# Optimization experiments

Measured on AMD Instinct MI355X. Metric: run time of the kernel, lower is better.

The kernel has to match this reference:

```python
import jax, jax.numpy as jnp
import numpy as np

LOG2 = float(np.log(2.0))


def setup_inputs() -> dict:
    key = jax.random.key(0)
    ks = jax.random.split(key, 10)
    V, G, F, T = 262144, 4096, 256, 2
    node_feats = jax.random.normal(ks[0], (V, F), dtype=jnp.float32)
    segment_ids = jnp.sort(jax.random.randint(ks[1], (V,), 0, G))
    s = 0.05
    return {
        "node_feats": node_feats,
        "segment_ids": segment_ids,
        "num_graphs": G,
        "logit_w": jax.random.normal(ks[2], (T, 2 * F, 1), dtype=jnp.float32) * s,
        "logit_b": jnp.zeros((T, 1), dtype=jnp.float32),
        "proj_w": jax.random.normal(ks[3], (T, F, F), dtype=jnp.float32) * s,
        "proj_b": jnp.zeros((T, F), dtype=jnp.float32),
        "gru_w_ih": jax.random.normal(ks[4], (T, 3 * F, F), dtype=jnp.float32) * s,
        "gru_w_hh": jax.random.normal(ks[5], (T, 3 * F, F), dtype=jnp.float32) * s,
        "gru_b_ih": jnp.zeros((T, 3 * F), dtype=jnp.float32),
        "gru_b_hh": jnp.zeros((T, 3 * F), dtype=jnp.float32),
    }


def _gru_cell(x, h, w_ih, w_hh, b_ih, b_hh):
    # torch.nn.GRUCell math
    gi = x @ w_ih.T + b_ih  # [G, 3F]
    gh = h @ w_hh.T + b_hh
    i_r, i_z, i_n = jnp.split(gi, 3, axis=-1)
    h_r, h_z, h_n = jnp.split(gh, 3, axis=-1)
    r = jax.nn.sigmoid(i_r + h_r)
    z = jax.nn.sigmoid(i_z + h_z)
    n = jnp.tanh(i_n + r * h_n)
    return (1.0 - z) * n + z * h


def reference(node_feats, segment_ids, num_graphs, logit_w, logit_b,
              proj_w, proj_b, gru_w_ih, gru_w_hh, gru_b_ih, gru_b_hh):
    G = int(num_graphs)
    # initial graph feats: sum of node feats per graph
    g_feats = jax.ops.segment_sum(node_feats, segment_ids, num_segments=G)
    T = logit_w.shape[0]
    for t in range(T):
        # broadcast relu(g_feats) to nodes, concat with node feats, compute logits
        ctx_nodes = jax.nn.relu(g_feats)[segment_ids]              # [V, F]
        z = jnp.concatenate([ctx_nodes, node_feats], axis=-1) @ logit_w[t] + logit_b[t]  # [V,1]
        z = jnp.logaddexp(z, 0.0) - LOG2                           # SoftPlus2
        # segment softmax over nodes within each graph
        zmax = jax.ops.segment_max(z, segment_ids, num_segments=G)
        e = jnp.exp(z - zmax[segment_ids])
        denom = jax.ops.segment_sum(e, segment_ids, num_segments=G)
        a = e / denom[segment_ids]                                 # [V,1]
        # project nodes (dropout=0) and attention-weighted sum per graph
        hv = node_feats @ proj_w[t] + proj_b[t]                    # [V, F]
        g_repr = jax.ops.segment_sum(a * hv, segment_ids, num_segments=G)
        context = jax.nn.elu(g_repr)
        g_feats = _gru_cell(context, g_feats, gru_w_ih[t], gru_w_hh[t], gru_b_ih[t], gru_b_hh[t])
    return g_feats
```

## Files before the change

### kernel.cpp

```cpp
#include <hip/hip_runtime.h>
#include <hip/hip_bf16.h>
#include <math.h>

#define V_NODES 262144
#define NGRAPH  4096
#define FD      256
#define TSTEPS  2
#define GP      16
#define SB      512
#define RS      264

typedef unsigned short u16;
typedef __attribute__((ext_vector_type(8))) short short8;
typedef __attribute__((ext_vector_type(4))) float f32x4;

__device__ __forceinline__ float bf2f(u16 u) {
  union { unsigned int i; float f; } x; x.i = ((unsigned int)u) << 16; return x.f;
}
__device__ __forceinline__ u16 f2bf(float f) {
  union { unsigned int i; float f; } x; x.f = f;
  unsigned int r = x.i + 0x7FFFu + ((x.i >> 16) & 1u);
  return (u16)(r >> 16);
}
__device__ __forceinline__ unsigned int pkbf(float a, float b) {
  return (unsigned int)f2bf(a) | ((unsigned int)f2bf(b) << 16);
}
__device__ __forceinline__ float softplus2(float x) {
  return fmaxf(x, 0.0f) + log1pf(__expf(-fabsf(x))) - 0.69314718056f;
}

__global__ __launch_bounds__(256) void k_prep(
    const int* __restrict__ seg, const float* __restrict__ w_ih,
    const float* __restrict__ w_hh, const float* __restrict__ proj_w,
    int* __restrict__ start, u16* __restrict__ wihbf, u16* __restrict__ whhbf,
    u16* __restrict__ whhlo, u16* __restrict__ pwtbf) {
  __shared__ float tl[32][33];
  const int b = blockIdx.x, tid = threadIdx.x;
  const int gtid = b * 256 + tid;
  {
    const int v = gtid;
    const int s = seg[v];
    if (v == 0) {
      for (int g = 0; g <= s; ++g) start[g] = 0;
    } else {
      const int p = seg[v - 1];
      for (int g = p + 1; g <= s; ++g) start[g] = v;
    }
    if (v == V_NODES - 1)
      for (int g = s + 1; g <= NGRAPH; ++g) start[g] = V_NODES;
  }
  {
    const int nchunk = TSTEPS * 768 * FD / 4;
    if (gtid < nchunk) {
      const float4 x = ((const float4*)w_ih)[gtid];
      uint2 u; u.x = pkbf(x.x, x.y); u.y = pkbf(x.z, x.w);
      ((uint2*)wihbf)[gtid] = u;
      const float4 y = ((const float4*)w_hh)[gtid];
      const u16 h0 = f2bf(y.x), h1 = f2bf(y.y), h2 = f2bf(y.z), h3 = f2bf(y.w);
      uint2 hi_, lo_;
      hi_.x = (unsigned)h0 | ((unsigned)h1 << 16);
      hi_.y = (unsigned)h2 | ((unsigned)h3 << 16);
      lo_.x = pkbf(y.x - bf2f(h0), y.y - bf2f(h1));
      lo_.y = pkbf(y.z - bf2f(h2), y.w - bf2f(h3));
      ((uint2*)whhbf)[gtid] = hi_;
      ((uint2*)whhlo)[gtid] = lo_;
    }
  }
  if (b < 2 * 64) {
    const int t = b >> 6, tile = b & 63, bx = tile & 7, by = tile >> 3;
    const int tx = tid & 31, ty = tid >> 5;
    const float* S = proj_w + (size_t)t * FD * FD;
    u16* D = pwtbf + (size_t)t * FD * FD;
#pragma unroll
    for (int i = 0; i < 32; i += 8)
      tl[ty + i][tx] = S[(size_t)(by * 32 + ty + i) * FD + bx * 32 + tx];
    __syncthreads();
#pragma unroll
    for (int i = 0; i < 32; i += 8)
      D[(size_t)(bx * 32 + ty + i) * FD + by * 32 + tx] = f2bf(tl[tx][ty + i]);
  }
}

__global__ __launch_bounds__(256) void k_pass1(
    const float* __restrict__ nf, const int* __restrict__ start,
    const float* __restrict__ logit_w, float* __restrict__ gf,
    u16* __restrict__ nbf, float* __restrict__ d0, float* __restrict__ d1) {
  __shared__ __align__(16) float redf[8][FD];
  const int g = blockIdx.x, tid = threadIdx.x;
  const int h = tid >> 5, sl = tid & 31;
  const int s = start[g], e = start[g + 1];
  float wA[8], wB[8];
  {
    const float4 a0 = ((const float4*)(logit_w + FD))[2 * sl];
    const float4 a1 = ((const float4*)(logit_w + FD))[2 * sl + 1];
    const float4 b0 = ((const float4*)(logit_w + 512 + FD))[2 * sl];
    const float4 b1 = ((const float4*)(logit_w + 512 + FD))[2 * sl + 1];
    wA[0]=a0.x; wA[1]=a0.y; wA[2]=a0.z; wA[3]=a0.w;
    wA[4]=a1.x; wA[5]=a1.y; wA[6]=a1.z; wA[7]=a1.w;
    wB[0]=b0.x; wB[1]=b0.y; wB[2]=b0.z; wB[3]=b0.w;
    wB[4]=b1.x; wB[5]=b1.y; wB[6]=b1.z; wB[7]=b1.w;
  }
  float ac[8];
#pragma unroll
  for (int j = 0; j < 8; ++j) ac[j] = 0.f;
  const float4* nfv = (const float4*)nf;
  for (int v = s + h; v < e; v += 8) {
    const float4 x0 = nfv[(size_t)v * 64 + 2 * sl];
    const float4 x1 = nfv[(size_t)v * 64 + 2 * sl + 1];
    ac[0]+=x0.x; ac[1]+=x0.y; ac[2]+=x0.z; ac[3]+=x0.w;
    ac[4]+=x1.x; ac[5]+=x1.y; ac[6]+=x1.z; ac[7]+=x1.w;
    uint4 u;
    u.x = pkbf(x0.x, x0.y); u.y = pkbf(x0.z, x0.w);
    u.z = pkbf(x1.x, x1.y); u.w = pkbf(x1.z, x1.w);
    ((uint4*)(nbf + (size_t)v * FD))[sl] = u;
    float dA = fmaf(x0.x, wA[0], fmaf(x0.y, wA[1], fmaf(x0.z, wA[2], x0.w * wA[3])));
    dA = fmaf(x1.x, wA[4], fmaf(x1.y, wA[5], fmaf(x1.z, wA[6], fmaf(x1.w, wA[7], dA))));
    float dB = fmaf(x0.x, wB[0], fmaf(x0.y, wB[1], fmaf(x0.z, wB[2], x0.w * wB[3])));
    dB = fmaf(x1.x, wB[4], fmaf(x1.y, wB[5], fmaf(x1.z, wB[6], fmaf(x1.w, wB[7], dB))));
#pragma unroll
    for (int off = 1; off < 32; off <<= 1) {
      dA += __shfl_xor(dA, off, 64);
      dB += __shfl_xor(dB, off, 64);
    }
    if (sl == 0) { d0[v] = dA; d1[v] = dB; }
  }
  ((float4*)&redf[h][sl * 8])[0] = make_float4(ac[0], ac[1], ac[2], ac[3]);
  ((float4*)&redf[h][sl * 8])[1] = make_float4(ac[4], ac[5], ac[6], ac[7]);
  __syncthreads();
  float sum = 0.f;
#pragma unroll
  for (int j = 0; j < 8; ++j) sum += redf[j][tid];
  gf[(size_t)g * FD + tid] = sum;
}

__global__ __launch_bounds__(SB, 1) void k_steps(
    const int* __restrict__ start, const float* __restrict__ logit_w,
    const float* __restrict__ logit_b, const float* __restrict__ proj_b,
    const float* __restrict__ b_ih, const float* __restrict__ b_hh,
    const u16* __restrict__ nbf, const float* __restrict__ d0,
    const float* __restrict__ d1, float* __restrict__ gf,
    float* __restrict__ gibuf, float* __restrict__ ghbuf,
    const u16* __restrict__ wihbf, const u16* __restrict__ whhbf,
    const u16* __restrict__ whhlo, const u16* __restrict__ pwtbf) {
  __shared__ __align__(16) float ew[2560];
  __shared__ __align__(16) float redf[GP * FD];
  __shared__ __align__(16) u16 wns_s[GP * RS];
  __shared__ __align__(16) u16 ctx_s[GP * RS];
  __shared__ __align__(16) u16 hhi_s[GP * RS];
  __shared__ __align__(16) u16 hlo_s[GP * RS];
  const int b = blockIdx.x, tid = threadIdx.x;
  const int lane = tid & 63, wv = tid >> 6;
  const int half = lane >> 5, sl = lane & 31;
  const int g0 = b * GP;
  const int vs = start[g0];
  const int hw = wv * 2 + half;
  const int g = g0 + hw;
  const int s = start[g], e = start[g + 1];

  for (int t = 0; t < TSTEPS; ++t) {
    for (int i = tid; i < GP * FD; i += SB) {
      const float x = gf[(size_t)g0 * FD + i];
      const u16 hb = f2bf(x);
      const int row = i >> 8, f = i & 255;
      hhi_s[row * RS + f] = hb;
      hlo_s[row * RS + f] = f2bf(x - bf2f(hb));
    }
    __syncthreads();
    {
      const float lb = logit_b[t];
      const float* dt = t ? d1 : d0;
      const float* lwA = logit_w + (size_t)t * 512;
      const float4 h0 = ((const float4*)(gf + (size_t)g * FD))[2 * sl];
      const float4 h1 = ((const float4*)(gf + (size_t)g * FD))[2 * sl + 1];
      const float4 wa0 = ((const float4*)lwA)[2 * sl];
      const float4 wa1 = ((const float4*)lwA)[2 * sl + 1];
      float c = fmaf(fmaxf(h0.x, 0.f), wa0.x, fmaf(fmaxf(h0.y, 0.f), wa0.y,
                fmaf(fmaxf(h0.z, 0.f), wa0.z, fmaxf(h0.w, 0.f) * wa0.w)));
      c = fmaf(fmaxf(h1.x, 0.f), wa1.x, fmaf(fmaxf(h1.y, 0.f), wa1.y,
          fmaf(fmaxf(h1.z, 0.f), wa1.z, fmaf(fmaxf(h1.w, 0.f), wa1.w, c))));
#pragma unroll
      for (int off = 1; off < 32; off <<= 1) c += __shfl_xor(c, off, 64);
      float m = -1e30f;
      for (int v = s + sl; v < e; v += 32) {
        const float z = softplus2(c + dt[v] + lb);
        ew[v - vs] = z;
        m = fmaxf(m, z);
      }
#pragma unroll
      for (int off = 1; off < 32; off <<= 1) m = fmaxf(m, __shfl_xor(m, off, 64));
      float ls = 0.f;
      for (int v = s + sl; v < e; v += 32) {
        const float ezz = __expf(ew[v - vs] - m);
        ew[v - vs] = ezz;
        ls += ezz;
      }
#pragma unroll
      for (int off = 1; off < 32; off <<= 1) ls += __shfl_xor(ls, off, 64);
      const float inv = (e > s) ? 1.0f / ls : 0.f;
      for (int v = s + sl; v < e; v += 32) ew[v - vs] *= inv;
      float acc[8];
#pragma unroll
      for (int j = 0; j < 8; ++j) acc[j] = 0.f;
      for (int v = s; v < e; ++v) {
        const uint4 u = ((const uint4*)(nbf + (size_t)v * FD))[sl];
        const float a = ew[v - vs];
        acc[0] = fmaf(a, bf2f((u16)(u.x & 0xffff)), acc[0]);
        acc[1] = fmaf(a, bf2f((u16)(u.x >> 16)),    acc[1]);
        acc[2] = fmaf(a, bf2f((u16)(u.y & 0xffff)), acc[2]);
        acc[3] = fmaf(a, bf2f((u16)(u.y >> 16)),    acc[3]);
        acc[4] = fmaf(a, bf2f((u16)(u.z & 0xffff)), acc[4]);
        acc[5] = fmaf(a, bf2f((u16)(u.z >> 16)),    acc[5]);
        acc[6] = fmaf(a, bf2f((u16)(u.w & 0xffff)), acc[6]);
        acc[7] = fmaf(a, bf2f((u16)(u.w >> 16)),    acc[7]);
      }
      ((float4*)&redf[hw * FD + sl * 8])[0] = make_float4(acc[0], acc[1], acc[2], acc[3]);
      ((float4*)&redf[hw * FD + sl * 8])[1] = make_float4(acc[4], acc[5], acc[6], acc[7]);
    }
    __syncthreads();
    for (int i = tid; i < GP * FD; i += SB)
      wns_s[(i >> 8) * RS + (i & 255)] = f2bf(redf[i]);
    __syncthreads();
    {
      const int r = lane & 15, q = lane >> 4;
      const u16* xp = wns_s + r * RS + q * 8;
#pragma unroll
      for (int jj = 0; jj < 2; ++jj) {
        const int nt = wv * 2 + jj;
        const u16* wp = pwtbf + (size_t)t * FD * FD + (size_t)(nt * 16 + r) * FD + q * 8;
        f32x4 a4 = {0.f, 0.f, 0.f, 0.f};
#pragma unroll
        for (int kt = 0; kt < 8; ++kt) {
          const short8 av = *(const short8*)(xp + kt * 32);
          const short8 bv = *(const short8*)(wp + kt * 32);
          a4 = __builtin_amdgcn_mfma_f32_16x16x32_bf16(av, bv, a4, 0, 0, 0);
        }
        const int gcol = nt * 16 + r;
        const float bs = proj_b[t * FD + gcol];
#pragma unroll
        for (int i = 0; i < 4; ++i) {
          float v = a4[i] + bs;
          v = (v > 0.0f) ? v : expm1f(v);
          ctx_s[(q * 4 + i) * RS + gcol] = f2bf(v);
        }
      }
    }
    __syncthreads();
    {
      const int r = lane & 15, q = lane >> 4;
      const u16* wih_t = wihbf + (size_t)t * 768 * FD;
      const u16* whh_t = whhbf + (size_t)t * 768 * FD;
      const u16* whl_t = whhlo + (size_t)t * 768 * FD;
      const u16* xi = ctx_s + r * RS + q * 8;
      const u16* xh = hhi_s + r * RS + q * 8;
      const u16* xl = hlo_s + r * RS + q * 8;
#pragma unroll
      for (int j = 0; j < 6; ++j) {
        const int nt = wv * 6 + j;
        const int gcol = nt * 16 + r;
        const u16* wi = wih_t + (size_t)gcol * FD + q * 8;
        const u16* wh = whh_t + (size_t)gcol * FD + q * 8;
        const u16* wl = whl_t + (size_t)gcol * FD + q * 8;
        f32x4 ai = {0.f, 0.f, 0.f, 0.f};
        f32x4 ah = {0.f, 0.f, 0.f, 0.f};
#pragma unroll
        for (int kt = 0; kt < 8; ++kt) {
          const short8 bi = *(const short8*)(wi + kt * 32);
          const short8 aiv = *(const short8*)(xi + kt * 32);
          ai = __builtin_amdgcn_mfma_f32_16x16x32_bf16(aiv, bi, ai, 0, 0, 0);
          const short8 bh = *(const short8*)(wh + kt * 32);
          const short8 xhh = *(const short8*)(xh + kt * 32);
          const short8 xll = *(const short8*)(xl + kt * 32);
          ah = __builtin_amdgcn_mfma_f32_16x16x32_bf16(xhh, bh, ah, 0, 0, 0);
          ah = __builtin_amdgcn_mfma_f32_16x16x32_bf16(xll, bh, ah, 0, 0, 0);
          const short8 bl = *(const short8*)(wl + kt * 32);
          ah = __builtin_amdgcn_mfma_f32_16x16x32_bf16(xhh, bl, ah, 0, 0, 0);
        }
        const float bi_ = b_ih[t * 768 + gcol];
        const float bh_ = b_hh[t * 768 + gcol];
#pragma unroll
        for (int i = 0; i < 4; ++i) {
          gibuf[(size_t)(g0 + q * 4 + i) * 768 + gcol] = ai[i] + bi_;
          ghbuf[(size_t)(g0 + q * 4 + i) * 768 + gcol] = ah[i] + bh_;
        }
      }
    }
    __syncthreads();
    for (int i = tid; i < GP * FD; i += SB) {
      const int lg = i >> 8, f = i & 255;
      const size_t gr = (size_t)(g0 + lg) * 768;
      const float ir = gibuf[gr + f], iz = gibuf[gr + 256 + f], in_ = gibuf[gr + 512 + f];
      const float hr = ghbuf[gr + f], hz = ghbuf[gr + 256 + f], hn = ghbuf[gr + 512 + f];
      const float rr = 1.0f / (1.0f + __expf(-(ir + hr)));
      const float zz = 1.0f / (1.0f + __expf(-(iz + hz)));
      const float nn = tanhf(in_ + rr * hn);
      const size_t idx = (size_t)g0 * FD + i;
      gf[idx] = (1.0f - zz) * nn + zz * gf[idx];
    }
    __syncthreads();
  }
}

extern "C" void kernel_launch(void* const* d_in, const int* in_sizes, int n_in,
                              void* d_out, int out_size, void* d_ws, size_t ws_size,
                              hipStream_t stream) {
  const float* node    = (const float*)d_in[0];
  const int*   seg     = (const int*)d_in[1];
  const float* logit_w = (const float*)d_in[3];
  const float* logit_b = (const float*)d_in[4];
  const float* proj_w  = (const float*)d_in[5];
  const float* proj_b  = (const float*)d_in[6];
  const float* w_ih    = (const float*)d_in[7];
  const float* w_hh    = (const float*)d_in[8];
  const float* b_ih    = (const float*)d_in[9];
  const float* b_hh    = (const float*)d_in[10];
  float* gfeats = (float*)d_out;

  char* p = (char*)d_ws;
  int* start   = (int*)p;   p += (((NGRAPH + 1) * sizeof(int)) + 255) & ~(size_t)255;
  u16* nbf     = (u16*)p;   p += (size_t)V_NODES * FD * 2;
  float* d0    = (float*)p; p += (size_t)V_NODES * 4;
  float* d1    = (float*)p; p += (size_t)V_NODES * 4;
  float* gi    = (float*)p; p += (size_t)NGRAPH * 768 * 4;
  float* gh    = (float*)p; p += (size_t)NGRAPH * 768 * 4;
  u16* wihbf   = (u16*)p;   p += (size_t)TSTEPS * 768 * FD * 2;
  u16* whhbf   = (u16*)p;   p += (size_t)TSTEPS * 768 * FD * 2;
  u16* whhlo   = (u16*)p;   p += (size_t)TSTEPS * 768 * FD * 2;
  u16* pwtbf   = (u16*)p;   p += (size_t)TSTEPS * FD * FD * 2;
  (void)ws_size; (void)in_sizes; (void)n_in; (void)out_size;

  k_prep<<<dim3(V_NODES / 256), dim3(256), 0, stream>>>(
      seg, w_ih, w_hh, proj_w, start, wihbf, whhbf, whhlo, pwtbf);
  k_pass1<<<dim3(NGRAPH), dim3(256), 0, stream>>>(
      node, start, logit_w, gfeats, nbf, d0, d1);
  k_steps<<<dim3(NGRAPH / GP), dim3(SB), 0, stream>>>(
      start, logit_w, logit_b, proj_b, b_ih, b_hh, nbf, d0, d1,
      gfeats, gi, gh, wihbf, whhbf, whhlo, pwtbf);
}
```

Before: 596.5 us.

## Fuse pass1 into step kernel, keep graph state and logits in LDS

Merges the node-sum/bf16-conversion pass into the step kernel so each block handles 8 graphs end to end. Graph features, per-node logit dot products and GRU results stay in shared memory instead of round-tripping through global d0/d1, gi/gh and gf buffers. The GRU gate elementwise math is fused directly into the MFMA epilogue, and node loops are unrolled by two. The group size is halved (MFMA rows padded with zeros) and occupancy raised, at the cost of wasted MFMA rows and a fixed LDS capacity for nodes per block.

```diff
diff --git a/kernel.cpp b/kernel.cpp
--- a/kernel.cpp
+++ b/kernel.cpp
@@ -6,9 +6,10 @@
 #define NGRAPH  4096
 #define FD      256
 #define TSTEPS  2
-#define GP      16
+#define GP      8
 #define SB      512
 #define RS      264
+#define EWCAP   1536
 
 typedef unsigned short u16;
 typedef __attribute__((ext_vector_type(8))) short short8;
@@ -27,6 +28,10 @@
 }
 __device__ __forceinline__ float softplus2(float x) {
   return fmaxf(x, 0.0f) + log1pf(__expf(-fabsf(x))) - 0.69314718056f;
+}
+__device__ __forceinline__ float dot8(const float4 x0, const float4 x1, const float* w) {
+  float d = fmaf(x0.x, w[0], fmaf(x0.y, w[1], fmaf(x0.z, w[2], x0.w * w[3])));
+  return fmaf(x1.x, w[4], fmaf(x1.y, w[5], fmaf(x1.z, w[6], fmaf(x1.w, w[7], d))));
 }
 
 __global__ __launch_bounds__(256) void k_prep(
@@ -81,144 +86,185 @@
   }
 }
 
-__global__ __launch_bounds__(256) void k_pass1(
+__global__ __launch_bounds__(SB, 4) void k_main(
     const float* __restrict__ nf, const int* __restrict__ start,
-    const float* __restrict__ logit_w, float* __restrict__ gf,
-    u16* __restrict__ nbf, float* __restrict__ d0, float* __restrict__ d1) {
-  __shared__ __align__(16) float redf[8][FD];
-  const int g = blockIdx.x, tid = threadIdx.x;
-  const int h = tid >> 5, sl = tid & 31;
-  const int s = start[g], e = start[g + 1];
-  float wA[8], wB[8];
-  {
-    const float4 a0 = ((const float4*)(logit_w + FD))[2 * sl];
-    const float4 a1 = ((const float4*)(logit_w + FD))[2 * sl + 1];
-    const float4 b0 = ((const float4*)(logit_w + 512 + FD))[2 * sl];
-    const float4 b1 = ((const float4*)(logit_w + 512 + FD))[2 * sl + 1];
-    wA[0]=a0.x; wA[1]=a0.y; wA[2]=a0.z; wA[3]=a0.w;
-    wA[4]=a1.x; wA[5]=a1.y; wA[6]=a1.z; wA[7]=a1.w;
-    wB[0]=b0.x; wB[1]=b0.y; wB[2]=b0.z; wB[3]=b0.w;
-    wB[4]=b1.x; wB[5]=b1.y; wB[6]=b1.z; wB[7]=b1.w;
-  }
-  float ac[8];
-#pragma unroll
-  for (int j = 0; j < 8; ++j) ac[j] = 0.f;
-  const float4* nfv = (const float4*)nf;
-  for (int v = s + h; v < e; v += 8) {
-    const float4 x0 = nfv[(size_t)v * 64 + 2 * sl];
-    const float4 x1 = nfv[(size_t)v * 64 + 2 * sl + 1];
-    ac[0]+=x0.x; ac[1]+=x0.y; ac[2]+=x0.z; ac[3]+=x0.w;
-    ac[4]+=x1.x; ac[5]+=x1.y; ac[6]+=x1.z; ac[7]+=x1.w;
-    uint4 u;
-    u.x = pkbf(x0.x, x0.y); u.y = pkbf(x0.z, x0.w);
-    u.z = pkbf(x1.x, x1.y); u.w = pkbf(x1.z, x1.w);
-    ((uint4*)(nbf + (size_t)v * FD))[sl] = u;
-    float dA = fmaf(x0.x, wA[0], fmaf(x0.y, wA[1], fmaf(x0.z, wA[2], x0.w * wA[3])));
-    dA = fmaf(x1.x, wA[4], fmaf(x1.y, wA[5], fmaf(x1.z, wA[6], fmaf(x1.w, wA[7], dA))));
-    float dB = fmaf(x0.x, wB[0], fmaf(x0.y, wB[1], fmaf(x0.z, wB[2], x0.w * wB[3])));
-    dB = fmaf(x1.x, wB[4], fmaf(x1.y, wB[5], fmaf(x1.z, wB[6], fmaf(x1.w, wB[7], dB))));
-#pragma unroll
-    for (int off = 1; off < 32; off <<= 1) {
-      dA += __shfl_xor(dA, off, 64);
-      dB += __shfl_xor(dB, off, 64);
-    }
-    if (sl == 0) { d0[v] = dA; d1[v] = dB; }
-  }
-  ((float4*)&redf[h][sl * 8])[0] = make_float4(ac[0], ac[1], ac[2], ac[3]);
-  ((float4*)&redf[h][sl * 8])[1] = make_float4(ac[4], ac[5], ac[6], ac[7]);
-  __syncthreads();
-  float sum = 0.f;
-#pragma unroll
-  for (int j = 0; j < 8; ++j) sum += redf[j][tid];
-  gf[(size_t)g * FD + tid] = sum;
-}
-
-__global__ __launch_bounds__(SB, 1) void k_steps(
-    const int* __restrict__ start, const float* __restrict__ logit_w,
-    const float* __restrict__ logit_b, const float* __restrict__ proj_b,
-    const float* __restrict__ b_ih, const float* __restrict__ b_hh,
-    const u16* __restrict__ nbf, const float* __restrict__ d0,
-    const float* __restrict__ d1, float* __restrict__ gf,
-    float* __restrict__ gibuf, float* __restrict__ ghbuf,
-    const u16* __restrict__ wihbf, const u16* __restrict__ whhbf,
-    const u16* __restrict__ whhlo, const u16* __restrict__ pwtbf) {
-  __shared__ __align__(16) float ew[2560];
-  __shared__ __align__(16) float redf[GP * FD];
-  __shared__ __align__(16) u16 wns_s[GP * RS];
-  __shared__ __align__(16) u16 ctx_s[GP * RS];
-  __shared__ __align__(16) u16 hhi_s[GP * RS];
-  __shared__ __align__(16) u16 hlo_s[GP * RS];
+    const float* __restrict__ logit_w, const float* __restrict__ logit_b,
+    const float* __restrict__ proj_b, const float* __restrict__ b_ih,
+    const float* __restrict__ b_hh, u16* __restrict__ nbf,
+    float* __restrict__ gf_out, const u16* __restrict__ wihbf,
+    const u16* __restrict__ whhbf, const u16* __restrict__ whhlo,
+    const u16* __restrict__ pwtbf) {
+  __shared__ __align__(16) float gf_s[GP][FD];
+  __shared__ __align__(16) float ew[EWCAP];
+  __shared__ __align__(16) float2 dle[EWCAP];
+  __shared__ __align__(16) u16 wns_s[16 * RS];
+  __shared__ __align__(16) u16 ctx_s[16 * RS];
+  __shared__ __align__(16) u16 hhi_s[16 * RS];
+  __shared__ __align__(16) u16 hlo_s[16 * RS];
+
   const int b = blockIdx.x, tid = threadIdx.x;
-  const int lane = tid & 63, wv = tid >> 6;
+  const int wv = tid >> 6, lane = tid & 63;
   const int half = lane >> 5, sl = lane & 31;
   const int g0 = b * GP;
+  const int g = g0 + wv;
   const int vs = start[g0];
-  const int hw = wv * 2 + half;
-  const int g = g0 + hw;
   const int s = start[g], e = start[g + 1];
+
+  for (int i = tid; i < 8 * RS; i += SB) {
+    wns_s[8 * RS + i] = 0; ctx_s[8 * RS + i] = 0;
+    hhi_s[8 * RS + i] = 0; hlo_s[8 * RS + i] = 0;
+  }
+
+  {
+    float wA[8], wB[8];
+    {
+      const float4 a0 = ((const float4*)(logit_w + FD))[2 * sl];
+      const float4 a1 = ((const float4*)(logit_w + FD))[2 * sl + 1];
+      const float4 b0 = ((const float4*)(logit_w + 512 + FD))[2 * sl];
+      const float4 b1 = ((const float4*)(logit_w + 512 + FD))[2 * sl + 1];
+      wA[0]=a0.x; wA[1]=a0.y; wA[2]=a0.z; wA[3]=a0.w;
+      wA[4]=a1.x; wA[5]=a1.y; wA[6]=a1.z; wA[7]=a1.w;
+      wB[0]=b0.x; wB[1]=b0.y; wB[2]=b0.z; wB[3]=b0.w;
+      wB[4]=b1.x; wB[5]=b1.y; wB[6]=b1.z; wB[7]=b1.w;
+    }
+    float ac[8];
+#pragma unroll
+    for (int j = 0; j < 8; ++j) ac[j] = 0.f;
+    const float4* nfv = (const float4*)nf;
+    int v = s + half;
+    for (; v + 2 < e; v += 4) {
+      const float4 x0 = nfv[(size_t)v * 64 + 2 * sl];
+      const float4 x1 = nfv[(size_t)v * 64 + 2 * sl + 1];
+      const float4 y0 = nfv[(size_t)(v + 2) * 64 + 2 * sl];
+      const float4 y1 = nfv[(size_t)(v + 2) * 64 + 2 * sl + 1];
+      uint4 u0, u1;
+      u0.x = pkbf(x0.x, x0.y); u0.y = pkbf(x0.z, x0.w);
+      u0.z = pkbf(x1.x, x1.y); u0.w = pkbf(x1.z, x1.w);
+      ((uint4*)(nbf + (size_t)v * FD))[sl] = u0;
+      u1.x = pkbf(y0.x, y0.y); u1.y = pkbf(y0.z, y0.w);
+      u1.z = pkbf(y1.x, y1.y); u1.w = pkbf(y1.z, y1.w);
+      ((uint4*)(nbf + (size_t)(v + 2) * FD))[sl] = u1;
+      ac[0] += x0.x + y0.x; ac[1] += x0.y + y0.y;
+      ac[2] += x0.z + y0.z; ac[3] += x0.w + y0.w;
+      ac[4] += x1.x + y1.x; ac[5] += x1.y + y1.y;
+      ac[6] += x1.z + y1.z; ac[7] += x1.w + y1.w;
+      float dA0 = dot8(x0, x1, wA), dB0 = dot8(x0, x1, wB);
+      float dA1 = dot8(y0, y1, wA), dB1 = dot8(y0, y1, wB);
+#pragma unroll
+      for (int off = 1; off < 32; off <<= 1) {
+        dA0 += __shfl_xor(dA0, off, 64); dB0 += __shfl_xor(dB0, off, 64);
+        dA1 += __shfl_xor(dA1, off, 64); dB1 += __shfl_xor(dB1, off, 64);
+      }
+      if (sl == 0) {
+        dle[v - vs] = make_float2(dA0, dB0);
+        dle[v + 2 - vs] = make_float2(dA1, dB1);
+      }
+    }
+    if (v < e) {
+      const float4 x0 = nfv[(size_t)v * 64 + 2 * sl];
+      const float4 x1 = nfv[(size_t)v * 64 + 2 * sl + 1];
+      uint4 u0;
+      u0.x = pkbf(x0.x, x0.y); u0.y = pkbf(x0.z, x0.w);
+      u0.z = pkbf(x1.x, x1.y); u0.w = pkbf(x1.z, x1.w);
+      ((uint4*)(nbf + (size_t)v * FD))[sl] = u0;
+      ac[0] += x0.x; ac[1] += x0.y; ac[2] += x0.z; ac[3] += x0.w;
+      ac[4] += x1.x; ac[5] += x1.y; ac[6] += x1.z; ac[7] += x1.w;
+      float dA0 = dot8(x0, x1, wA), dB0 = dot8(x0, x1, wB);
+#pragma unroll
+      for (int off = 1; off < 32; off <<= 1) {
+        dA0 += __shfl_xor(dA0, off, 64); dB0 += __shfl_xor(dB0, off, 64);
+      }
+      if (sl == 0) dle[v - vs] = make_float2(dA0, dB0);
+    }
+#pragma unroll
+    for (int j = 0; j < 8; ++j) ac[j] += __shfl_xor(ac[j], 32, 64);
+    if (half == 0) {
+      ((float4*)&gf_s[wv][sl * 8])[0] = make_float4(ac[0], ac[1], ac[2], ac[3]);
+      ((float4*)&gf_s[wv][sl * 8])[1] = make_float4(ac[4], ac[5], ac[6], ac[7]);
+    }
+  }
+  __syncthreads();
 
   for (int t = 0; t < TSTEPS; ++t) {
     for (int i = tid; i < GP * FD; i += SB) {
-      const float x = gf[(size_t)g0 * FD + i];
+      const float x = gf_s[i >> 8][i & 255];
       const u16 hb = f2bf(x);
-      const int row = i >> 8, f = i & 255;
-      hhi_s[row * RS + f] = hb;
-      hlo_s[row * RS + f] = f2bf(x - bf2f(hb));
-    }
-    __syncthreads();
+      hhi_s[(i >> 8) * RS + (i & 255)] = hb;
+      hlo_s[(i >> 8) * RS + (i & 255)] = f2bf(x - bf2f(hb));
+    }
     {
       const float lb = logit_b[t];
-      const float* dt = t ? d1 : d0;
-      const float* lwA = logit_w + (size_t)t * 512;
-      const float4 h0 = ((const float4*)(gf + (size_t)g * FD))[2 * sl];
-      const float4 h1 = ((const float4*)(gf + (size_t)g * FD))[2 * sl + 1];
-      const float4 wa0 = ((const float4*)lwA)[2 * sl];
-      const float4 wa1 = ((const float4*)lwA)[2 * sl + 1];
-      float c = fmaf(fmaxf(h0.x, 0.f), wa0.x, fmaf(fmaxf(h0.y, 0.f), wa0.y,
-                fmaf(fmaxf(h0.z, 0.f), wa0.z, fmaxf(h0.w, 0.f) * wa0.w)));
-      c = fmaf(fmaxf(h1.x, 0.f), wa1.x, fmaf(fmaxf(h1.y, 0.f), wa1.y,
-          fmaf(fmaxf(h1.z, 0.f), wa1.z, fmaf(fmaxf(h1.w, 0.f), wa1.w, c))));
-#pragma unroll
-      for (int off = 1; off < 32; off <<= 1) c += __shfl_xor(c, off, 64);
+      const float4 h4 = ((const float4*)&gf_s[wv][0])[lane];
+      const float4 w4 = ((const float4*)(logit_w + (size_t)t * 512))[lane];
+      float c = fmaf(fmaxf(h4.x, 0.f), w4.x, fmaf(fmaxf(h4.y, 0.f), w4.y,
+                fmaf(fmaxf(h4.z, 0.f), w4.z, fmaxf(h4.w, 0.f) * w4.w)));
+#pragma unroll
+      for (int off = 1; off < 64; off <<= 1) c += __shfl_xor(c, off, 64);
       float m = -1e30f;
-      for (int v = s + sl; v < e; v += 32) {
-        const float z = softplus2(c + dt[v] + lb);
-        ew[v - vs] = z;
+      for (int v2 = s + lane; v2 < e; v2 += 64) {
+        const float2 dd = dle[v2 - vs];
+        const float z = softplus2(c + (t ? dd.y : dd.x) + lb);
+        ew[v2 - vs] = z;
         m = fmaxf(m, z);
       }
 #pragma unroll
-      for (int off = 1; off < 32; off <<= 1) m = fmaxf(m, __shfl_xor(m, off, 64));
+      for (int off = 1; off < 64; off <<= 1) m = fmaxf(m, __shfl_xor(m, off, 64));
       float ls = 0.f;
-      for (int v = s + sl; v < e; v += 32) {
-        const float ezz = __expf(ew[v - vs] - m);
-        ew[v - vs] = ezz;
-        ls += ezz;
-      }
-#pragma unroll
-      for (int off = 1; off < 32; off <<= 1) ls += __shfl_xor(ls, off, 64);
+      for (int v2 = s + lane; v2 < e; v2 += 64) {
+        const float ez = __expf(ew[v2 - vs] - m);
+        ew[v2 - vs] = ez;
+        ls += ez;
+      }
+#pragma unroll
+      for (int off = 1; off < 64; off <<= 1) ls += __shfl_xor(ls, off, 64);
       const float inv = (e > s) ? 1.0f / ls : 0.f;
-      for (int v = s + sl; v < e; v += 32) ew[v - vs] *= inv;
+      for (int v2 = s + lane; v2 < e; v2 += 64) ew[v2 - vs] *= inv;
       float acc[8];
 #pragma unroll
       for (int j = 0; j < 8; ++j) acc[j] = 0.f;
-      for (int v = s; v < e; ++v) {
-        const uint4 u = ((const uint4*)(nbf + (size_t)v * FD))[sl];
-        const float a = ew[v - vs];
-        acc[0] = fmaf(a, bf2f((u16)(u.x & 0xffff)), acc[0]);
-        acc[1] = fmaf(a, bf2f((u16)(u.x >> 16)),    acc[1]);
-        acc[2] = fmaf(a, bf2f((u16)(u.y & 0xffff)), acc[2]);
-        acc[3] = fmaf(a, bf2f((u16)(u.y >> 16)),    acc[3]);
-        acc[4] = fmaf(a, bf2f((u16)(u.z & 0xffff)), acc[4]);
-        acc[5] = fmaf(a, bf2f((u16)(u.z >> 16)),    acc[5]);
-        acc[6] = fmaf(a, bf2f((u16)(u.w & 0xffff)), acc[6]);
-        acc[7] = fmaf(a, bf2f((u16)(u.w >> 16)),    acc[7]);
-      }
-      ((float4*)&redf[hw * FD + sl * 8])[0] = make_float4(acc[0], acc[1], acc[2], acc[3]);
-      ((float4*)&redf[hw * FD + sl * 8])[1] = make_float4(acc[4], acc[5], acc[6], acc[7]);
-    }
-    __syncthreads();
-    for (int i = tid; i < GP * FD; i += SB)
-      wns_s[(i >> 8) * RS + (i & 255)] = f2bf(redf[i]);
+      int v = s + half;
+      for (; v + 2 < e; v += 4) {
+        const uint4 u0 = ((const uint4*)(nbf + (size_t)v * FD))[sl];
+        const uint4 u1 = ((const uint4*)(nbf + (size_t)(v + 2) * FD))[sl];
+        const float a0 = ew[v - vs], a1 = ew[v + 2 - vs];
+        acc[0] = fmaf(a0, bf2f((u16)(u0.x & 0xffff)), acc[0]);
+        acc[1] = fmaf(a0, bf2f((u16)(u0.x >> 16)),    acc[1]);
+        acc[2] = fmaf(a0, bf2f((u16)(u0.y & 0xffff)), acc[2]);
+        acc[3] = fmaf(a0, bf2f((u16)(u0.y >> 16)),    acc[3]);
+        acc[4] = fmaf(a0, bf2f((u16)(u0.z & 0xffff)), acc[4]);
+        acc[5] = fmaf(a0, bf2f((u16)(u0.z >> 16)),    acc[5]);
+        acc[6] = fmaf(a0, bf2f((u16)(u0.w & 0xffff)), acc[6]);
+        acc[7] = fmaf(a0, bf2f((u16)(u0.w >> 16)),    acc[7]);
+        acc[0] = fmaf(a1, bf2f((u16)(u1.x & 0xffff)), acc[0]);
+        acc[1] = fmaf(a1, bf2f((u16)(u1.x >> 16)),    acc[1]);
+        acc[2] = fmaf(a1, bf2f((u16)(u1.y & 0xffff)), acc[2]);
+        acc[3] = fmaf(a1, bf2f((u16)(u1.y >> 16)),    acc[3]);
+        acc[4] = fmaf(a1, bf2f((u16)(u1.z & 0xffff)), acc[4]);
+        acc[5] = fmaf(a1, bf2f((u16)(u1.z >> 16)),    acc[5]);
+        acc[6] = fmaf(a1, bf2f((u16)(u1.w & 0xffff)), acc[6]);
+        acc[7] = fmaf(a1, bf2f((u16)(u1.w >> 16)),    acc[7]);
+      }
+      if (v < e) {
+        const uint4 u0 = ((const uint4*)(nbf + (size_t)v * FD))[sl];
+        const float a0 = ew[v - vs];
+        acc[0] = fmaf(a0, bf2f((u16)(u0.x & 0xffff)), acc[0]);
+        acc[1] = fmaf(a0, bf2f((u16)(u0.x >> 16)),    acc[1]);
+        acc[2] = fmaf(a0, bf2f((u16)(u0.y & 0xffff)), acc[2]);
+        acc[3] = fmaf(a0, bf2f((u16)(u0.y >> 16)),    acc[3]);
+        acc[4] = fmaf(a0, bf2f((u16)(u0.z & 0xffff)), acc[4]);
+        acc[5] = fmaf(a0, bf2f((u16)(u0.z >> 16)),    acc[5]);
+        acc[6] = fmaf(a0, bf2f((u16)(u0.w & 0xffff)), acc[6]);
+        acc[7] = fmaf(a0, bf2f((u16)(u0.w >> 16)),    acc[7]);
+      }
+#pragma unroll
+      for (int j = 0; j < 8; ++j) acc[j] += __shfl_xor(acc[j], 32, 64);
+      if (half == 0) {
+        uint4 w;
+        w.x = pkbf(acc[0], acc[1]); w.y = pkbf(acc[2], acc[3]);
+        w.z = pkbf(acc[4], acc[5]); w.w = pkbf(acc[6], acc[7]);
+        *(uint4*)(wns_s + wv * RS + sl * 8) = w;
+      }
+    }
     __syncthreads();
     {
       const int r = lane & 15, q = lane >> 4;
@@ -238,66 +284,83 @@
         const float bs = proj_b[t * FD + gcol];
 #pragma unroll
         for (int i = 0; i < 4; ++i) {
-          float v = a4[i] + bs;
-          v = (v > 0.0f) ? v : expm1f(v);
-          ctx_s[(q * 4 + i) * RS + gcol] = f2bf(v);
+          float vv = a4[i] + bs;
+          vv = (vv > 0.0f) ? vv : expm1f(vv);
+          ctx_s[(q * 4 + i) * RS + gcol] = f2bf(vv);
         }
       }
     }
     __syncthreads();
     {
       const int r = lane & 15, q = lane >> 4;
+      const u16* xi = ctx_s + r * RS + q * 8;
+      const u16* xh = hhi_s + r * RS + q * 8;
+      const u16* xl = hlo_s + r * RS + q * 8;
       const u16* wih_t = wihbf + (size_t)t * 768 * FD;
       const u16* whh_t = whhbf + (size_t)t * 768 * FD;
       const u16* whl_t = whhlo + (size_t)t * 768 * FD;
-      const u16* xi = ctx_s + r * RS + q * 8;
-      const u16* xh = hhi_s + r * RS + q * 8;
-      const u16* xl = hlo_s + r * RS + q * 8;
-#pragma unroll
-      for (int j = 0; j < 6; ++j) {
-        const int nt = wv * 6 + j;
-        const int gcol = nt * 16 + r;
-        const u16* wi = wih_t + (size_t)gcol * FD + q * 8;
-        const u16* wh = whh_t + (size_t)gcol * FD + q * 8;
-        const u16* wl = whl_t + (size_t)gcol * FD + q * 8;
-        f32x4 ai = {0.f, 0.f, 0.f, 0.f};
-        f32x4 ah = {0.f, 0.f, 0.f, 0.f};
+      auto gpair = [&](const u16* wi, const u16* wh, const u16* wl,
+                       f32x4& ai, f32x4& ah) {
 #pragma unroll
         for (int kt = 0; kt < 8; ++kt) {
-          const short8 bi = *(const short8*)(wi + kt * 32);
           const short8 aiv = *(const short8*)(xi + kt * 32);
+          const short8 bi  = *(const short8*)(wi + kt * 32);
           ai = __builtin_amdgcn_mfma_f32_16x16x32_bf16(aiv, bi, ai, 0, 0, 0);
-          const short8 bh = *(const short8*)(wh + kt * 32);
           const short8 xhh = *(const short8*)(xh + kt * 32);
           const short8 xll = *(const short8*)(xl + kt * 32);
+          const short8 bh  = *(const short8*)(wh + kt * 32);
+          const short8 bl  = *(const short8*)(wl + kt * 32);
           ah = __builtin_amdgcn_mfma_f32_16x16x32_bf16(xhh, bh, ah, 0, 0, 0);
           ah = __builtin_amdgcn_mfma_f32_16x16x32_bf16(xll, bh, ah, 0, 0, 0);
-          const short8 bl = *(const short8*)(wl + kt * 32);
           ah = __builtin_amdgcn_mfma_f32_16x16x32_bf16(xhh, bl, ah, 0, 0, 0);
         }
-        const float bi_ = b_ih[t * 768 + gcol];
-        const float bh_ = b_hh[t * 768 + gcol];
-#pragma unroll
-        for (int i = 0; i < 4; ++i) {
-          gibuf[(size_t)(g0 + q * 4 + i) * 768 + gcol] = ai[i] + bi_;
-          ghbuf[(size_t)(g0 + q * 4 + i) * 768 + gcol] = ah[i] + bh_;
+      };
+#pragma unroll
+      for (int jj = 0; jj < 2; ++jj) {
+        const int col = (wv * 2 + jj) * 16 + r;
+        float rr[4], zz[4];
+        {
+          f32x4 ai = {0.f,0.f,0.f,0.f}, ah = {0.f,0.f,0.f,0.f};
+          gpair(wih_t + (size_t)col * FD + q * 8,
+                whh_t + (size_t)col * FD + q * 8,
+                whl_t + (size_t)col * FD + q * 8, ai, ah);
+          const float bi_ = b_ih[t * 768 + col], bh_ = b_hh[t * 768 + col];
+#pragma unroll
+          for (int i = 0; i < 4; ++i)
+            rr[i] = 1.f / (1.f + __expf(-(ai[i] + bi_ + ah[i] + bh_)));
+        }
+        {
+          f32x4 ai = {0.f,0.f,0.f,0.f}, ah = {0.f,0.f,0.f,0.f};
+          gpair(wih_t + (size_t)(256 + col) * FD + q * 8,
+                whh_t + (size_t)(256 + col) * FD + q * 8,
+                whl_t + (size_t)(256 + col) * FD + q * 8, ai, ah);
+          const float bi_ = b_ih[t * 768 + 256 + col], bh_ = b_hh[t * 768 + 256 + col];
+#pragma unroll
+          for (int i = 0; i < 4; ++i)
+            zz[i] = 1.f / (1.f + __expf(-(ai[i] + bi_ + ah[i] + bh_)));
+        }
+        {
+          f32x4 ai = {0.f,0.f,0.f,0.f}, ah = {0.f,0.f,0.f,0.f};
+          gpair(wih_t + (size_t)(512 + col) * FD + q * 8,
+                whh_t + (size_t)(512 + col) * FD + q * 8,
+                whl_t + (size_t)(512 + col) * FD + q * 8, ai, ah);
+          const float bi_ = b_ih[t * 768 + 512 + col], bh_ = b_hh[t * 768 + 512 + col];
+          if (q < 2) {
+#pragma unroll
+            for (int i = 0; i < 4; ++i) {
+              const int row = q * 4 + i;
+              const float nn = tanhf(ai[i] + bi_ + rr[i] * (ah[i] + bh_));
+              const float hold = gf_s[row][col];
+              gf_s[row][col] = (1.f - zz[i]) * nn + zz[i] * hold;
+            }
+          }
         }
       }
     }
     __syncthreads();
-    for (int i = tid; i < GP * FD; i += SB) {
-      const int lg = i >> 8, f = i & 255;
-      const size_t gr = (size_t)(g0 + lg) * 768;
-      const float ir = gibuf[gr + f], iz = gibuf[gr + 256 + f], in_ = gibuf[gr + 512 + f];
-      const float hr = ghbuf[gr + f], hz = ghbuf[gr + 256 + f], hn = ghbuf[gr + 512 + f];
-      const float rr = 1.0f / (1.0f + __expf(-(ir + hr)));
-      const float zz = 1.0f / (1.0f + __expf(-(iz + hz)));
-      const float nn = tanhf(in_ + rr * hn);
-      const size_t idx = (size_t)g0 * FD + i;
-      gf[idx] = (1.0f - zz) * nn + zz * gf[idx];
-    }
-    __syncthreads();
-  }
+  }
+
+  ((float4*)(gf_out + (size_t)g0 * FD))[tid] = ((const float4*)gf_s)[tid];
 }
 
 extern "C" void kernel_launch(void* const* d_in, const int* in_sizes, int n_in,
@@ -318,10 +381,6 @@
   char* p = (char*)d_ws;
   int* start   = (int*)p;   p += (((NGRAPH + 1) * sizeof(int)) + 255) & ~(size_t)255;
   u16* nbf     = (u16*)p;   p += (size_t)V_NODES * FD * 2;
-  float* d0    = (float*)p; p += (size_t)V_NODES * 4;
-  float* d1    = (float*)p; p += (size_t)V_NODES * 4;
-  float* gi    = (float*)p; p += (size_t)NGRAPH * 768 * 4;
-  float* gh    = (float*)p; p += (size_t)NGRAPH * 768 * 4;
   u16* wihbf   = (u16*)p;   p += (size_t)TSTEPS * 768 * FD * 2;
   u16* whhbf   = (u16*)p;   p += (size_t)TSTEPS * 768 * FD * 2;
   u16* whhlo   = (u16*)p;   p += (size_t)TSTEPS * 768 * FD * 2;
@@ -330,9 +389,7 @@
 
   k_prep<<<dim3(V_NODES / 256), dim3(256), 0, stream>>>(
       seg, w_ih, w_hh, proj_w, start, wihbf, whhbf, whhlo, pwtbf);
-  k_pass1<<<dim3(NGRAPH), dim3(256), 0, stream>>>(
-      node, start, logit_w, gfeats, nbf, d0, d1);
-  k_steps<<<dim3(NGRAPH / GP), dim3(SB), 0, stream>>>(
-      start, logit_w, logit_b, proj_b, b_ih, b_hh, nbf, d0, d1,
-      gfeats, gi, gh, wihbf, whhbf, whhlo, pwtbf);
-}
+  k_main<<<dim3(NGRAPH / GP), dim3(SB), 0, stream>>>(
+      node, start, logit_w, logit_b, proj_b, b_ih, b_hh, nbf, gfeats,
+      wihbf, whhbf, whhlo, pwtbf);
+}
```

New measurement: 658.1 us. 10.3% more time.
